# Performance work log

Measured on AMD Instinct MI355X. Metric: run time of the kernel, lower is better.

Reference implementation:

```python
import jax, jax.numpy as jnp
import numpy as np

D_MODEL, NHEAD = 256, 8
HEAD_DIM = D_MODEL // NHEAD  # 32, also the conv group count


def layer_norm(x, w, b, eps=1e-5):
    mu = jnp.mean(x, axis=-1, keepdims=True)
    var = jnp.var(x, axis=-1, keepdims=True)
    return (x - mu) * jax.lax.rsqrt(var + eps) * w + b


def setup_inputs() -> dict:
    key = jax.random.key(0)
    ks = jax.random.split(key, 12)
    b, H, W = 4, 120, 160
    L = H * W  # 19200; 'self' path requires L == H*W
    d, h = D_MODEL, NHEAD
    s = 0.05
    p = lambda i, shape: jax.random.normal(ks[i], shape, jnp.float32) * s
    return {
        "x": jax.random.normal(ks[0], (b, L, d), jnp.float32),
        "source": jax.random.normal(ks[1], (b, L, d), jnp.float32),
        "Wq": p(2, (d, d)), "Wk": p(3, (d, d)), "Wv": p(4, (d, d)),
        "Wmerge": p(5, (d, d)),
        "Wmlp1": p(6, (2 * d, 2 * d)), "Wmlp2": p(7, (2 * d, d)),
        "ln1_w": jnp.ones((d,), jnp.float32), "ln1_b": jnp.zeros((d,), jnp.float32),
        "ln2_w": jnp.ones((d,), jnp.float32), "ln2_b": jnp.zeros((d,), jnp.float32),
        "Wdown": p(8, (2 * d, 64)), "Wup": p(9, (64, d)),
        "fc_w": p(10, (9, 3 * h)), "fc_b": jnp.zeros((9,), jnp.float32),
        "dep_w": p(11, (d, 9, 3, 3)),  # torch OIHW layout, groups=32 (O/g=8, I/g=9)
        "dep_b": jnp.zeros((d,), jnp.float32),
        "rate": jnp.full((1,), 0.5, jnp.float32),
        "H": H, "W": W,
    }


def reference(x, source, Wq, Wk, Wv, Wmerge, Wmlp1, Wmlp2,
              ln1_w, ln1_b, ln2_w, ln2_b, Wdown, Wup,
              fc_w, fc_b, dep_w, dep_b, rate, H, W):
    # name == 'self' path is hardcoded (conv branch active)
    b, L, d = x.shape
    h, hd = NHEAD, HEAD_DIM
    S = source.shape[1]

    q = (x @ Wq).reshape(b, L, h, hd)
    k = (source @ Wk).reshape(b, S, h, hd)
    v = (source @ Wv).reshape(b, S, h, hd)

    # ---- conv branch ----
    # [b, L, h, 3*hd] -> [b, L, 3h, hd] -> [b, 3h, L, hd]
    f_all = jnp.concatenate([q, k, v], axis=-1).reshape(b, L, 3 * h, hd)
    f_all = jnp.transpose(f_all, (0, 2, 1, 3))
    # 1x1 conv 3h -> 9 over (L, hd) 'spatial' grid
    f9 = jnp.einsum('oc,bcld->bold', fc_w, f_all) + fc_b[None, :, None, None]
    # [b, 9, L, hd] -> [b, hd, 9, L] -> [b, 9*hd, H, W]
    f_conv = jnp.transpose(f9, (0, 3, 1, 2)).reshape(b, 9 * hd, H, W)
    out_conv = jax.lax.conv_general_dilated(
        f_conv, dep_w, window_strides=(1, 1), padding=((1, 1), (1, 1)),
        feature_group_count=hd, dimension_numbers=('NCHW', 'OIHW', 'NCHW'))
    out_conv = out_conv + dep_b[None, :, None, None]
    out_conv = jnp.transpose(out_conv, (0, 2, 3, 1)).reshape(b, L, d)

    # ---- linear attention (elu+1 feature map), O(N) ----
    Qf = jax.nn.elu(q) + 1.0
    Kf = jax.nn.elu(k) + 1.0
    v_len = jnp.float32(S)
    vals = v / v_len
    KV = jnp.einsum('bshd,bshv->bhdv', Kf, vals)
    Z = 1.0 / (jnp.einsum('blhd,bhd->blh', Qf, Kf.sum(axis=1)) + 1e-6)
    message = jnp.einsum('blhd,bhdv,blh->blhv', Qf, KV, Z) * v_len

    # ---- merge / norm / MLP / adapter ----
    message = message.reshape(b, L, d) @ Wmerge
    message = layer_norm(message, ln1_w, ln1_b)
    cat1 = jnp.concatenate([x, message], axis=2)
    message = jax.nn.relu(cat1 @ Wmlp1) @ Wmlp2
    message = layer_norm(message, ln2_w, ln2_b)

    cat2 = jnp.concatenate([x, message], axis=2)
    up = jax.nn.relu(cat2 @ Wdown) @ Wup
    message = message + up * 0.1
    message = message + rate * out_conv
    return x + message
```

## Files before the change

kernel.cpp:

```cpp
#include <hip/hip_runtime.h>
#include <stdint.h>

#define LL 19200
#define NBATCH 4
#define NROWS (NBATCH * LL)
#define HH 120
#define WW 160

typedef short bhalf8 __attribute__((ext_vector_type(8)));
typedef float f32x4 __attribute__((ext_vector_type(4)));

__device__ __forceinline__ float bfbits2f(uint32_t u) { union { uint32_t i; float f; } c; c.i = u << 16; return c.f; }
__device__ __forceinline__ float bf2f(uint16_t h) { return bfbits2f((uint32_t)h); }
__device__ __forceinline__ uint16_t f2bf(float f) {
    union { float f; uint32_t i; } c; c.f = f;
    return (uint16_t)((c.i + 0x7FFFu + ((c.i >> 16) & 1u)) >> 16);
}
__device__ __forceinline__ uint32_t pk2(uint16_t a, uint16_t b) { return (uint32_t)a | ((uint32_t)b << 16); }
__device__ __forceinline__ float elup1(float x) { return x > 0.f ? x + 1.f : expf(x); }

__device__ __forceinline__ uint4 pack8f(const float* p) {
    float4 lo = *(const float4*)p; float4 hi = *(const float4*)(p + 4);
    uint4 s;
    s.x = pk2(f2bf(lo.x), f2bf(lo.y)); s.y = pk2(f2bf(lo.z), f2bf(lo.w));
    s.z = pk2(f2bf(hi.x), f2bf(hi.y)); s.w = pk2(f2bf(hi.z), f2bf(hi.w));
    return s;
}

__device__ __forceinline__ void gll16(const void* g, void* l) {
    __builtin_amdgcn_global_load_lds((const __attribute__((address_space(1))) uint32_t*)g,
                                     (__attribute__((address_space(3))) uint32_t*)l, 16, 0, 0);
}

__global__ __launch_bounds__(256)
void prep_all(const float* __restrict__ Wq, const float* __restrict__ Wk,
              const float* __restrict__ Wv, const float* __restrict__ Wm,
              const float* __restrict__ Wm1, const float* __restrict__ Wm2,
              const float* __restrict__ Wd, const float* __restrict__ Wu,
              uint16_t* __restrict__ wq, uint16_t* __restrict__ wk,
              uint16_t* __restrict__ wvv, uint16_t* __restrict__ wm,
              uint16_t* __restrict__ wm1, uint16_t* __restrict__ wm2,
              uint16_t* __restrict__ wd, uint16_t* __restrict__ wu) {
    int blk = blockIdx.x;
    const float* s; uint16_t* d; int K, N, base;
    if (blk < 1024) {
        int which = blk >> 8; base = which << 8;
        s = which == 0 ? Wq : which == 1 ? Wk : which == 2 ? Wv : Wm;
        d = which == 0 ? wq : which == 1 ? wk : which == 2 ? wvv : wm;
        K = 256; N = 256;
    } else if (blk < 2048) { s = Wm1; d = wm1; K = 512; N = 512; base = 1024; }
    else if (blk < 2560)   { s = Wm2; d = wm2; K = 512; N = 256; base = 2048; }
    else if (blk < 2688)   { s = Wd;  d = wd;  K = 512; N = 64;  base = 2560; }
    else                   { s = Wu;  d = wu;  K = 64;  N = 256; base = 2688; }
    int idx = (blk - base) * 256 + threadIdx.x;
    int n = idx / K, kk = idx - n * K;
    d[idx] = f2bf(s[(long)kk * N + n]);
}

#define EPI_NONE 0
#define EPI_RELU 1
#define EPI_LN 2
#define EPI_FINAL 3

template<int BN, int MODE_A, int EPI>
__global__ __launch_bounds__(512)
void gemm_big(const float* __restrict__ A0f, const uint16_t* __restrict__ A0b,
              const uint16_t* __restrict__ A1b,
              const uint16_t* __restrict__ Wt, int K,
              uint16_t* __restrict__ outb, float* __restrict__ outf, int outW,
              uint16_t* __restrict__ sideout,
              const float* __restrict__ lnw, const float* __restrict__ lnb,
              const float* __restrict__ xres, const uint16_t* __restrict__ xresb,
              const uint16_t* __restrict__ msg2res,
              const uint16_t* __restrict__ convres, const float* __restrict__ ratep)
{
    constexpr int WCOLS = BN / 64;
    constexpr int WROWS = 8 / WCOLS;
    constexpr int MT = 128 / (WROWS * 16);
    __shared__ __align__(16) uint16_t a_sm[128 * 32];
    __shared__ __align__(16) uint16_t b_sm[BN * 32];
    const int tid = threadIdx.x;
    const int lane = tid & 63;
    const int wv = tid >> 6;
    const int wr = wv / WCOLS, wc = wv % WCOLS;
    const long row0 = (long)blockIdx.x * 128;
    const int col0 = blockIdx.y * BN;

    f32x4 acc[MT][4];
#pragma unroll
    for (int m = 0; m < MT; ++m)
#pragma unroll
        for (int n = 0; n < 4; ++n) acc[m][n] = (f32x4){0.f, 0.f, 0.f, 0.f};

    const int sr = tid >> 2;
    const int sc = (tid & 3) * 8;
    const long argA = row0 + sr;
    uint16_t* a_dst = a_sm + wv * 512;
    uint16_t* b_dst = b_sm + wv * 512;

    for (int k0 = 0; k0 < K; k0 += 32) {
        if (MODE_A == 0) {
            gll16(A0b + argA * (long)K + k0 + sc, a_dst);
        } else if (MODE_A == 1) {
            uint4 stg = pack8f(A0f + argA * (long)K + k0 + sc);
            *(uint4*)&a_sm[sr * 32 + sc] = stg;
            if (sideout) *(uint4*)(sideout + argA * (long)K + k0 + sc) = stg;
        } else if (MODE_A == 2) {
            if (k0 < 256) *(uint4*)&a_sm[sr * 32 + sc] = pack8f(A0f + argA * 256 + k0 + sc);
            else          gll16(A1b + argA * 256 + (k0 - 256) + sc, a_dst);
        } else {
            const uint16_t* srcp = (k0 < 256) ? (A0b + argA * 256 + k0 + sc)
                                              : (A1b + argA * 256 + (k0 - 256) + sc);
            gll16(srcp, a_dst);
        }
        if (BN == 256) {
            gll16(Wt + (long)(col0 + sr) * K + k0 + sc, b_dst);
            gll16(Wt + (long)(col0 + 128 + sr) * K + k0 + sc, b_sm + 4096 + wv * 512);
        } else {
            if (tid < 256) gll16(Wt + (long)(col0 + sr) * K + k0 + sc, b_dst);
        }
        __syncthreads();
        bhalf8 af[MT];
#pragma unroll
        for (int m = 0; m < MT; ++m)
            af[m] = *(const bhalf8*)&a_sm[(wr * MT * 16 + m * 16 + (lane & 15)) * 32 + (lane >> 4) * 8];
#pragma unroll
        for (int n = 0; n < 4; ++n) {
            bhalf8 bfr = *(const bhalf8*)&b_sm[(wc * 64 + n * 16 + (lane & 15)) * 32 + (lane >> 4) * 8];
#pragma unroll
            for (int m = 0; m < MT; ++m)
                acc[m][n] = __builtin_amdgcn_mfma_f32_16x16x32_bf16(af[m], bfr, acc[m][n], 0, 0, 0);
        }
        __syncthreads();
    }

    const int cl = lane & 15;
    const int rg4 = (lane >> 4) * 4;

    if constexpr (EPI == EPI_LN) {
        __shared__ float red_s[4][128];
        __shared__ float red_ss[4][128];
#pragma unroll
        for (int m = 0; m < MT; ++m)
#pragma unroll
            for (int j = 0; j < 4; ++j) {
                float p = 0.f, pp = 0.f;
#pragma unroll
                for (int n = 0; n < 4; ++n) { float v = acc[m][n][j]; p += v; pp += v * v; }
#pragma unroll
                for (int msk = 1; msk < 16; msk <<= 1) { p += __shfl_xor(p, msk, 64); pp += __shfl_xor(pp, msk, 64); }
                if (cl == 0) {
                    int lr = wr * 64 + m * 16 + rg4 + j;
                    red_s[wc][lr] = p; red_ss[wc][lr] = pp;
                }
            }
        __syncthreads();
#pragma unroll
        for (int m = 0; m < MT; ++m)
#pragma unroll
            for (int j = 0; j < 4; ++j) {
                int lr = wr * 64 + m * 16 + rg4 + j;
                float s = red_s[0][lr] + red_s[1][lr] + red_s[2][lr] + red_s[3][lr];
                float ss = red_ss[0][lr] + red_ss[1][lr] + red_ss[2][lr] + red_ss[3][lr];
                float mu = s * (1.f / 256.f);
                float var = ss * (1.f / 256.f) - mu * mu;
                float rstd = rsqrtf(var + 1e-5f);
                long rowg = row0 + lr;
#pragma unroll
                for (int n = 0; n < 4; ++n) {
                    int col = wc * 64 + n * 16 + cl;
                    float vv = (acc[m][n][j] - mu) * rstd * lnw[col] + lnb[col];
                    outb[rowg * (long)outW + col] = f2bf(vv);
                }
            }
    } else if constexpr (EPI == EPI_FINAL) {
        float rate = ratep[0];
#pragma unroll
        for (int m = 0; m < MT; ++m)
#pragma unroll
            for (int j = 0; j < 4; ++j) {
                long rowg = row0 + wr * MT * 16 + m * 16 + rg4 + j;
                int bb = (int)(rowg / LL);
                int ll = (int)(rowg - (long)bb * LL);
#pragma unroll
                for (int n = 0; n < 4; ++n) {
                    int col = wc * 64 + n * 16 + cl;
                    long o = rowg * 256 + col;
                    float xv = xresb ? bf2f(xresb[o]) : xres[o];
                    float m2 = bf2f(msg2res[o]);
                    float cv = bf2f(convres[((long)(bb * 256 + col)) * LL + ll]);
                    outf[o] = xv + m2 + 0.1f * acc[m][n][j] + rate * cv;
                }
            }
    } else {
#pragma unroll
        for (int m = 0; m < MT; ++m)
#pragma unroll
            for (int j = 0; j < 4; ++j) {
                long rowg = row0 + wr * MT * 16 + m * 16 + rg4 + j;
#pragma unroll
                for (int n = 0; n < 4; ++n) {
                    int col = col0 + wc * 64 + n * 16 + cl;
                    float vv = acc[m][n][j];
                    if (EPI == EPI_RELU) vv = vv > 0.f ? vv : 0.f;
                    outb[rowg * (long)outW + col] = f2bf(vv);
                }
            }
    }
}

__global__ __launch_bounds__(256)
void kv_partial(const uint16_t* __restrict__ kb, const uint16_t* __restrict__ vb,
                float* __restrict__ part) {
    __shared__ float kf_sm[32][33];
    __shared__ float v_sm[32][36];
    const int tid = threadIdx.x;
    const int bh = blockIdx.y, b = bh >> 3, h = bh & 7;
    const int s0 = blockIdx.x * 256;
    const int d = tid >> 3, vg = tid & 7;
    const int sl = tid >> 3, e4 = (tid & 7) * 4;
    float a0 = 0.f, a1 = 0.f, a2 = 0.f, a3 = 0.f, aKs = 0.f;
    for (int it = 0; it < 8; ++it) {
        long base = ((long)(b * LL + s0 + it * 32 + sl)) * 256 + h * 32 + e4;
        uint2 kk = *(const uint2*)(kb + base);
        uint2 vv = *(const uint2*)(vb + base);
        kf_sm[sl][e4 + 0] = elup1(bfbits2f(kk.x & 0xFFFFu));
        kf_sm[sl][e4 + 1] = elup1(bfbits2f(kk.x >> 16));
        kf_sm[sl][e4 + 2] = elup1(bfbits2f(kk.y & 0xFFFFu));
        kf_sm[sl][e4 + 3] = elup1(bfbits2f(kk.y >> 16));
        float4 vf;
        vf.x = bfbits2f(vv.x & 0xFFFFu); vf.y = bfbits2f(vv.x >> 16);
        vf.z = bfbits2f(vv.y & 0xFFFFu); vf.w = bfbits2f(vv.y >> 16);
        *(float4*)&v_sm[sl][e4] = vf;
        __syncthreads();
#pragma unroll 8
        for (int s = 0; s < 32; ++s) {
            float kf = kf_sm[s][d];
            aKs += kf;
            float4 v4 = *(const float4*)&v_sm[s][vg * 4];
            a0 += kf * v4.x; a1 += kf * v4.y; a2 += kf * v4.z; a3 += kf * v4.w;
        }
        __syncthreads();
    }
    long pb = ((long)(blockIdx.x * 32 + bh)) * 1056;
    part[pb + d * 32 + vg * 4 + 0] = a0;
    part[pb + d * 32 + vg * 4 + 1] = a1;
    part[pb + d * 32 + vg * 4 + 2] = a2;
    part[pb + d * 32 + vg * 4 + 3] = a3;
    if (vg == 0) part[pb + 1024 + d] = aKs;
}

__global__ __launch_bounds__(256)
void kv_final(const float* __restrict__ part, float* __restrict__ KVg, float* __restrict__ Ksum) {
    const int bh = blockIdx.x, tid = threadIdx.x;
    for (int idx = tid; idx < 1056; idx += 256) {
        float s = 0.f;
        for (int c = 0; c < 75; ++c) s += part[((long)(c * 32 + bh)) * 1056 + idx];
        if (idx < 1024) KVg[bh * 1024 + idx] = s;
        else Ksum[bh * 32 + idx - 1024] = s;
    }
}

__global__ __launch_bounds__(256)
void attn_mfma(const uint16_t* __restrict__ qb, const float* __restrict__ KVg,
               const float* __restrict__ Ksum, uint16_t* __restrict__ msgout) {
    const int tid = threadIdx.x;
    const int lane = tid & 63;
    const int wv = tid >> 6;
    const long l0 = (long)blockIdx.x * 64;
    const int b = (int)(l0 / LL);
    const int l15 = lane & 15, lk = lane >> 4;
#pragma unroll
    for (int hi = 0; hi < 2; ++hi) {
        const int h = wv * 2 + hi;
        const float* kvb = KVg + ((long)(b * 8 + h)) * 1024;
        const float* ksb = Ksum + (b * 8 + h) * 32;
        bhalf8 B0, B1;
        float ks[8];
#pragma unroll
        for (int i = 0; i < 8; ++i) {
            int k = lk * 8 + i;
            B0[i] = (short)f2bf(kvb[k * 32 + l15]);
            B1[i] = (short)f2bf(kvb[k * 32 + 16 + l15]);
            ks[i] = ksb[k];
        }
#pragma unroll
        for (int rt = 0; rt < 4; ++rt) {
            long row = l0 + rt * 16 + l15;
            uint4 qv = *(const uint4*)(qb + row * 256 + h * 32 + lk * 8);
            float qf[8];
            qf[0] = elup1(bfbits2f(qv.x & 0xFFFFu)); qf[1] = elup1(bfbits2f(qv.x >> 16));
            qf[2] = elup1(bfbits2f(qv.y & 0xFFFFu)); qf[3] = elup1(bfbits2f(qv.y >> 16));
            qf[4] = elup1(bfbits2f(qv.z & 0xFFFFu)); qf[5] = elup1(bfbits2f(qv.z >> 16));
            qf[6] = elup1(bfbits2f(qv.w & 0xFFFFu)); qf[7] = elup1(bfbits2f(qv.w >> 16));
            bhalf8 A;
#pragma unroll
            for (int i = 0; i < 8; ++i) A[i] = (short)f2bf(qf[i]);
            float p = qf[0]*ks[0] + qf[1]*ks[1] + qf[2]*ks[2] + qf[3]*ks[3]
                    + qf[4]*ks[4] + qf[5]*ks[5] + qf[6]*ks[6] + qf[7]*ks[7];
            p += __shfl_xor(p, 16, 64);
            p += __shfl_xor(p, 32, 64);
            f32x4 d0 = (f32x4){0.f,0.f,0.f,0.f}, d1 = (f32x4){0.f,0.f,0.f,0.f};
            d0 = __builtin_amdgcn_mfma_f32_16x16x32_bf16(A, B0, d0, 0, 0, 0);
            d1 = __builtin_amdgcn_mfma_f32_16x16x32_bf16(A, B1, d1, 0, 0, 0);
#pragma unroll
            for (int j = 0; j < 4; ++j) {
                int orl = lk * 4 + j;
                float zr = __shfl(p, orl, 64);
                float Z = 1.f / (zr + 1e-6f);
                long orow = l0 + rt * 16 + orl;
                msgout[orow * 256 + h * 32 + l15]      = f2bf(d0[j] * Z);
                msgout[orow * 256 + h * 32 + 16 + l15] = f2bf(d1[j] * Z);
            }
        }
    }
}

__global__ __launch_bounds__(256)
void f9_kernel(const uint16_t* __restrict__ qb, const uint16_t* __restrict__ kb,
               const uint16_t* __restrict__ vb, const float* __restrict__ fcw,
               const float* __restrict__ fcb, uint16_t* __restrict__ fconv) {
    __shared__ __align__(16) uint16_t sm[3 * 32 * 256];
    char* smb = (char*)sm;
    const int tid = threadIdx.x;
    const int b = blockIdx.y;
    const int l0 = blockIdx.x * 32;
    for (int idx = tid; idx < 3072; idx += 256) {
        int tsr = idx >> 10, row = (idx >> 5) & 31, c = idx & 31;
        const uint16_t* src = tsr == 0 ? qb : (tsr == 1 ? kb : vb);
        uint4 v = *(const uint4*)(src + ((long)(b * LL + l0 + row)) * 256 + c * 8);
        int boff = (c * 16) ^ ((row & 7) << 4);
        *(uint4*)(smb + (tsr * 32 + row) * 512 + boff) = v;
    }
    __syncthreads();
    const int li = tid & 31, g = tid >> 5;
    float acc[9][4];
#pragma unroll
    for (int o = 0; o < 9; ++o) {
        float bv = fcb[o];
#pragma unroll
        for (int j = 0; j < 4; ++j) acc[o][j] = bv;
    }
    const int swz = (li & 7) << 4;
#pragma unroll
    for (int h = 0; h < 8; ++h) {
        float f[3][4];
#pragma unroll
        for (int s = 0; s < 3; ++s) {
            int boff = (h * 64 + g * 8) ^ swz;
            uint2 r = *(const uint2*)(smb + (s * 32 + li) * 512 + boff);
            f[s][0] = bfbits2f(r.x & 0xFFFFu); f[s][1] = bfbits2f(r.x >> 16);
            f[s][2] = bfbits2f(r.y & 0xFFFFu); f[s][3] = bfbits2f(r.y >> 16);
        }
#pragma unroll
        for (int o = 0; o < 9; ++o) {
            float w0 = fcw[o * 24 + 3 * h + 0];
            float w1 = fcw[o * 24 + 3 * h + 1];
            float w2 = fcw[o * 24 + 3 * h + 2];
#pragma unroll
            for (int j = 0; j < 4; ++j)
                acc[o][j] += w0 * f[0][j] + w1 * f[1][j] + w2 * f[2][j];
        }
    }
    const long ob = (long)(b * 288) * LL + l0 + li;
#pragma unroll
    for (int j = 0; j < 4; ++j) {
        int dp = g * 4 + j;
#pragma unroll
        for (int o = 0; o < 9; ++o)
            fconv[ob + (long)(dp * 9 + o) * LL] = f2bf(acc[o][j]);
    }
}

__global__ __launch_bounds__(256)
void dwconv2(const uint16_t* __restrict__ fconv, const float* __restrict__ depw,
             const float* __restrict__ depb, uint16_t* __restrict__ convout) {
    __shared__ __align__(16) uint16_t in_sm[9][26][48];
    __shared__ float w_sm[8][81];
    __shared__ float b_sm2[8];
    const int tid = threadIdx.x;
    const int bg = blockIdx.z, b = bg >> 5, g = bg & 31;
    const int y0 = blockIdx.y * 24;
    const int x0 = blockIdx.x * 32;
    for (int idx = tid; idx < 648; idx += 256)
        w_sm[idx / 81][idx % 81] = depw[(long)(g * 8) * 81 + idx];
    if (tid < 8) b_sm2[tid] = depb[g * 8 + tid];
    for (int rIdx = tid; rIdx < 234; rIdx += 256) {
        int i = rIdx / 26, r = rIdx - i * 26;
        int yy = y0 + r - 1;
        uint16_t* dst = &in_sm[i][r][0];
        if (yy >= 0 && yy < HH) {
            const uint16_t* rp = fconv + ((long)(b * 288 + g * 9 + i)) * LL + yy * WW;
            *(uint4*)&dst[8]  = *(const uint4*)(rp + x0);
            *(uint4*)&dst[16] = *(const uint4*)(rp + x0 + 8);
            *(uint4*)&dst[24] = *(const uint4*)(rp + x0 + 16);
            *(uint4*)&dst[32] = *(const uint4*)(rp + x0 + 24);
            dst[7]  = (x0 > 0) ? rp[x0 - 1] : (uint16_t)0;
            dst[40] = (x0 + 32 < WW) ? rp[x0 + 32] : (uint16_t)0;
        } else {
            uint4 z = {0, 0, 0, 0};
            *(uint4*)&dst[8] = z; *(uint4*)&dst[16] = z;
            *(uint4*)&dst[24] = z; *(uint4*)&dst[32] = z;
            dst[7] = 0; dst[40] = 0;
        }
    }
    __syncthreads();
    const int xi = tid & 7, m = (tid >> 3) & 7, ys = tid >> 6;
    float acc[6][4];
    float bias = b_sm2[m];
#pragma unroll
    for (int r = 0; r < 6; ++r)
#pragma unroll
        for (int o = 0; o < 4; ++o) acc[r][o] = bias;
    for (int i = 0; i < 9; ++i) {
        float w[9];
#pragma unroll
        for (int t = 0; t < 9; ++t) w[t] = w_sm[m][i * 9 + t];
#pragma unroll
        for (int rr = 0; rr < 8; ++rr) {
            const uint16_t* rowb = &in_sm[i][ys * 6 + rr][4 + xi * 4];
            uint2 lo = *(const uint2*)rowb;
            uint2 hi = *(const uint2*)(rowb + 4);
            uint32_t ex = *(const uint32_t*)(rowb + 8);
            float f[6];
            f[0] = bfbits2f(lo.y >> 16);
            f[1] = bfbits2f(hi.x & 0xFFFFu);
            f[2] = bfbits2f(hi.x >> 16);
            f[3] = bfbits2f(hi.y & 0xFFFFu);
            f[4] = bfbits2f(hi.y >> 16);
            f[5] = bfbits2f(ex & 0xFFFFu);
#pragma unroll
            for (int ky = 0; ky < 3; ++ky) {
                int ro = rr - ky;
                if (ro >= 0 && ro < 6) {
#pragma unroll
                    for (int o = 0; o < 4; ++o)
                        acc[ro][o] += w[ky * 3 + 0] * f[o] + w[ky * 3 + 1] * f[o + 1] + w[ky * 3 + 2] * f[o + 2];
                }
            }
        }
    }
    long chbase = ((long)(b * 256 + g * 8 + m)) * LL;
#pragma unroll
    for (int rl = 0; rl < 6; ++rl) {
        int y = y0 + ys * 6 + rl;
        uint2 st;
        st.x = pk2(f2bf(acc[rl][0]), f2bf(acc[rl][1]));
        st.y = pk2(f2bf(acc[rl][2]), f2bf(acc[rl][3]));
        *(uint2*)(convout + chbase + (long)y * WW + x0 + xi * 4) = st;
    }
}

extern "C" void kernel_launch(void* const* d_in, const int* in_sizes, int n_in,
                              void* d_out, int out_size, void* d_ws, size_t ws_size,
                              hipStream_t stream) {
    (void)in_sizes; (void)n_in; (void)out_size;
    const float* x      = (const float*)d_in[0];
    const float* src    = (const float*)d_in[1];
    const float* Wq     = (const float*)d_in[2];
    const float* Wk     = (const float*)d_in[3];
    const float* Wv     = (const float*)d_in[4];
    const float* Wmerge = (const float*)d_in[5];
    const float* Wmlp1  = (const float*)d_in[6];
    const float* Wmlp2  = (const float*)d_in[7];
    const float* ln1w   = (const float*)d_in[8];
    const float* ln1b   = (const float*)d_in[9];
    const float* ln2w   = (const float*)d_in[10];
    const float* ln2b   = (const float*)d_in[11];
    const float* Wdown  = (const float*)d_in[12];
    const float* Wup    = (const float*)d_in[13];
    const float* fcw    = (const float*)d_in[14];
    const float* fcb    = (const float*)d_in[15];
    const float* depw   = (const float*)d_in[16];
    const float* depb   = (const float*)d_in[17];
    const float* rate   = (const float*)d_in[18];

    char* ws = (char*)d_ws;
    const size_t SZ_NB = (size_t)NROWS * 256 * 2;
    const size_t O_Q = 0;
    const size_t O_K = SZ_NB;
    const size_t O_V = 2 * SZ_NB;
    const size_t O_FCONV = 3 * SZ_NB;
    const size_t O_CONVOUT = O_FCONV + (size_t)NBATCH * 288 * LL * 2;
    const size_t O_PART = O_CONVOUT + SZ_NB;
    const size_t O_KV = O_PART + (size_t)75 * 32 * 1056 * 4;
    const size_t O_KS = O_KV + (size_t)32 * 1024 * 4;
    const size_t O_WT = O_KS + (size_t)32 * 32 * 4;
    const size_t O_XB = O_WT + 704512 * 2 + 1024;
    const size_t O_SRCB = O_XB + SZ_NB;
    const size_t NEED = O_SRCB + SZ_NB;

    uint16_t* qB      = (uint16_t*)(ws + O_Q);
    uint16_t* kB      = (uint16_t*)(ws + O_K);
    uint16_t* vB      = (uint16_t*)(ws + O_V);
    uint16_t* fconv   = (uint16_t*)(ws + O_FCONV);
    uint16_t* convout = (uint16_t*)(ws + O_CONVOUT);
    float*    part    = (float*)(ws + O_PART);
    float*    KVg     = (float*)(ws + O_KV);
    float*    Ksg     = (float*)(ws + O_KS);
    uint16_t* wt_q    = (uint16_t*)(ws + O_WT);
    uint16_t* wt_k    = wt_q + 256 * 256;
    uint16_t* wt_v    = wt_k + 256 * 256;
    uint16_t* wt_m    = wt_v + 256 * 256;
    uint16_t* wt_m1   = wt_m + 256 * 256;
    uint16_t* wt_m2   = wt_m1 + 512 * 512;
    uint16_t* wt_d    = wt_m2 + 512 * 256;
    uint16_t* wt_u    = wt_d + 512 * 64;
    uint16_t* xb      = (uint16_t*)(ws + O_XB);
    uint16_t* srcb    = (uint16_t*)(ws + O_SRCB);
    uint16_t* msgattn = kB;
    uint16_t* msgB    = vB;
    uint16_t* hidden  = qB;
    uint16_t* msg2    = fconv;
    uint16_t* h2      = (uint16_t*)(ws + O_PART);

    const bool big = ws_size >= NEED;

    prep_all<<<2752, 256, 0, stream>>>(Wq, Wk, Wv, Wmerge, Wmlp1, Wmlp2, Wdown, Wup,
                                       wt_q, wt_k, wt_v, wt_m, wt_m1, wt_m2, wt_d, wt_u);

    const dim3 g600(NROWS / 128, 1);
    gemm_big<256, 1, EPI_NONE><<<g600, 512, 0, stream>>>(x, nullptr, nullptr, wt_q, 256, qB, nullptr, 256,
        big ? xb : nullptr, nullptr, nullptr, nullptr, nullptr, nullptr, nullptr, nullptr);
    gemm_big<256, 1, EPI_NONE><<<g600, 512, 0, stream>>>(src, nullptr, nullptr, wt_k, 256, kB, nullptr, 256,
        big ? srcb : nullptr, nullptr, nullptr, nullptr, nullptr, nullptr, nullptr, nullptr);
    if (big) {
        gemm_big<256, 0, EPI_NONE><<<g600, 512, 0, stream>>>(nullptr, srcb, nullptr, wt_v, 256, vB, nullptr, 256,
            nullptr, nullptr, nullptr, nullptr, nullptr, nullptr, nullptr, nullptr);
    } else {
        gemm_big<256, 1, EPI_NONE><<<g600, 512, 0, stream>>>(src, nullptr, nullptr, wt_v, 256, vB, nullptr, 256,
            nullptr, nullptr, nullptr, nullptr, nullptr, nullptr, nullptr, nullptr);
    }
    kv_partial<<<dim3(75, 32), 256, 0, stream>>>(kB, vB, part);
    kv_final<<<32, 256, 0, stream>>>(part, KVg, Ksg);
    f9_kernel<<<dim3(LL / 32, NBATCH), 256, 0, stream>>>(qB, kB, vB, fcw, fcb, fconv);
    dwconv2<<<dim3(5, 5, 128), 256, 0, stream>>>(fconv, depw, depb, convout);
    attn_mfma<<<NROWS / 64, 256, 0, stream>>>(qB, KVg, Ksg, msgattn);
    gemm_big<256, 0, EPI_LN><<<g600, 512, 0, stream>>>(nullptr, msgattn, nullptr, wt_m, 256, msgB, nullptr, 256,
        nullptr, ln1w, ln1b, nullptr, nullptr, nullptr, nullptr, nullptr);
    if (big) {
        gemm_big<256, 3, EPI_RELU><<<dim3(NROWS / 128, 2), 512, 0, stream>>>(nullptr, xb, msgB, wt_m1, 512, hidden, nullptr, 512,
            nullptr, nullptr, nullptr, nullptr, nullptr, nullptr, nullptr, nullptr);
    } else {
        gemm_big<256, 2, EPI_RELU><<<dim3(NROWS / 128, 2), 512, 0, stream>>>(x, nullptr, msgB, wt_m1, 512, hidden, nullptr, 512,
            nullptr, nullptr, nullptr, nullptr, nullptr, nullptr, nullptr, nullptr);
    }
    gemm_big<256, 0, EPI_LN><<<g600, 512, 0, stream>>>(nullptr, hidden, nullptr, wt_m2, 512, msg2, nullptr, 256,
        nullptr, ln2w, ln2b, nullptr, nullptr, nullptr, nullptr, nullptr);
    if (big) {
        gemm_big<64, 3, EPI_RELU><<<g600, 512, 0, stream>>>(nullptr, xb, msg2, wt_d, 512, h2, nullptr, 64,
            nullptr, nullptr, nullptr, nullptr, nullptr, nullptr, nullptr, nullptr);
    } else {
        gemm_big<64, 2, EPI_RELU><<<g600, 512, 0, stream>>>(x, nullptr, msg2, wt_d, 512, h2, nullptr, 64,
            nullptr, nullptr, nullptr, nullptr, nullptr, nullptr, nullptr, nullptr);
    }
    gemm_big<256, 0, EPI_FINAL><<<g600, 512, 0, stream>>>(nullptr, h2, nullptr, wt_u, 64, nullptr, (float*)d_out, 256,
        nullptr, nullptr, nullptr, x, big ? xb : nullptr, msg2, convout, rate);
}
```

Measured before the change: 835.3 us.

## Double-buffer GEMM LDS tiles, template K, and tile-transpose weight prep

The GEMM main loop now keeps two LDS buffers, so the next k-slice's global-to-LDS loads are issued before the current slice's MFMAs and one barrier per iteration is removed. K becomes a template parameter so the k-loop can be fully unrolled and address arithmetic folded. Weight preparation switches from a strided per-element transpose over 2752 blocks to a 64x64 shared-memory tiled transpose over 172 blocks, giving coalesced reads and writes. Doubling LDS per block may lower occupancy, and the larger unrolled code may raise register pressure.

```diff
diff --git a/kernel.cpp b/kernel.cpp
--- a/kernel.cpp
+++ b/kernel.cpp
@@ -41,20 +41,32 @@
               uint16_t* __restrict__ wvv, uint16_t* __restrict__ wm,
               uint16_t* __restrict__ wm1, uint16_t* __restrict__ wm2,
               uint16_t* __restrict__ wd, uint16_t* __restrict__ wu) {
+    __shared__ float ts[64][65];
+    const int tid = threadIdx.x;
     int blk = blockIdx.x;
-    const float* s; uint16_t* d; int K, N, base;
-    if (blk < 1024) {
-        int which = blk >> 8; base = which << 8;
-        s = which == 0 ? Wq : which == 1 ? Wk : which == 2 ? Wv : Wm;
-        d = which == 0 ? wq : which == 1 ? wk : which == 2 ? wvv : wm;
-        K = 256; N = 256;
-    } else if (blk < 2048) { s = Wm1; d = wm1; K = 512; N = 512; base = 1024; }
-    else if (blk < 2560)   { s = Wm2; d = wm2; K = 512; N = 256; base = 2048; }
-    else if (blk < 2688)   { s = Wd;  d = wd;  K = 512; N = 64;  base = 2560; }
-    else                   { s = Wu;  d = wu;  K = 64;  N = 256; base = 2688; }
-    int idx = (blk - base) * 256 + threadIdx.x;
-    int n = idx / K, kk = idx - n * K;
-    d[idx] = f2bf(s[(long)kk * N + n]);
+    const float* s; uint16_t* d; int K, N, t;
+    if (blk < 64)        { int w = blk >> 4; t = blk & 15;
+                           s = w == 0 ? Wq : w == 1 ? Wk : w == 2 ? Wv : Wm;
+                           d = w == 0 ? wq : w == 1 ? wk : w == 2 ? wvv : wm;
+                           K = 256; N = 256; }
+    else if (blk < 128)  { s = Wm1; d = wm1; K = 512; N = 512; t = blk - 64; }
+    else if (blk < 160)  { s = Wm2; d = wm2; K = 512; N = 256; t = blk - 128; }
+    else if (blk < 168)  { s = Wd;  d = wd;  K = 512; N = 64;  t = blk - 160; }
+    else                 { s = Wu;  d = wu;  K = 64;  N = 256; t = blk - 168; }
+    const int ntk = K >> 6;
+    const int tn = t / ntk, tk = t - tn * ntk;
+    const int c = tid & 63, r4 = tid >> 6;
+#pragma unroll
+    for (int i = 0; i < 16; ++i) {
+        int r = r4 * 16 + i;
+        ts[r][c] = s[(long)(tk * 64 + r) * N + tn * 64 + c];
+    }
+    __syncthreads();
+#pragma unroll
+    for (int i = 0; i < 16; ++i) {
+        int rr = r4 * 16 + i;
+        d[(long)(tn * 64 + rr) * K + tk * 64 + c] = f2bf(ts[c][rr]);
+    }
 }
 
 #define EPI_NONE 0
@@ -62,11 +74,11 @@
 #define EPI_LN 2
 #define EPI_FINAL 3
 
-template<int BN, int MODE_A, int EPI>
+template<int BN, int K, int MODE_A, int EPI>
 __global__ __launch_bounds__(512)
 void gemm_big(const float* __restrict__ A0f, const uint16_t* __restrict__ A0b,
               const uint16_t* __restrict__ A1b,
-              const uint16_t* __restrict__ Wt, int K,
+              const uint16_t* __restrict__ Wt,
               uint16_t* __restrict__ outb, float* __restrict__ outf, int outW,
               uint16_t* __restrict__ sideout,
               const float* __restrict__ lnw, const float* __restrict__ lnb,
@@ -77,14 +89,17 @@
     constexpr int WCOLS = BN / 64;
     constexpr int WROWS = 8 / WCOLS;
     constexpr int MT = 128 / (WROWS * 16);
-    __shared__ __align__(16) uint16_t a_sm[128 * 32];
-    __shared__ __align__(16) uint16_t b_sm[BN * 32];
+    constexpr int ASZ = 128 * 32;
+    constexpr int BSZ = BN * 32;
+    __shared__ __align__(16) uint16_t a_sm[2 * ASZ];
+    __shared__ __align__(16) uint16_t b_sm[2 * BSZ];
     const int tid = threadIdx.x;
     const int lane = tid & 63;
     const int wv = tid >> 6;
     const int wr = wv / WCOLS, wc = wv % WCOLS;
     const long row0 = (long)blockIdx.x * 128;
     const int col0 = blockIdx.y * BN;
+    const int l15 = lane & 15, lk = lane >> 4;
 
     f32x4 acc[MT][4];
 #pragma unroll
@@ -95,47 +110,62 @@
     const int sr = tid >> 2;
     const int sc = (tid & 3) * 8;
     const long argA = row0 + sr;
-    uint16_t* a_dst = a_sm + wv * 512;
-    uint16_t* b_dst = b_sm + wv * 512;
-
-    for (int k0 = 0; k0 < K; k0 += 32) {
+
+    auto stageAB = [&](int buf, int k0) {
+        uint16_t* ab = a_sm + buf * ASZ;
+        uint16_t* bb = b_sm + buf * BSZ;
         if (MODE_A == 0) {
-            gll16(A0b + argA * (long)K + k0 + sc, a_dst);
+            gll16(A0b + argA * (long)K + k0 + sc, ab + wv * 512);
         } else if (MODE_A == 1) {
             uint4 stg = pack8f(A0f + argA * (long)K + k0 + sc);
-            *(uint4*)&a_sm[sr * 32 + sc] = stg;
+            *(uint4*)&ab[sr * 32 + sc] = stg;
             if (sideout) *(uint4*)(sideout + argA * (long)K + k0 + sc) = stg;
         } else if (MODE_A == 2) {
-            if (k0 < 256) *(uint4*)&a_sm[sr * 32 + sc] = pack8f(A0f + argA * 256 + k0 + sc);
-            else          gll16(A1b + argA * 256 + (k0 - 256) + sc, a_dst);
+            if (k0 < 256) *(uint4*)&ab[sr * 32 + sc] = pack8f(A0f + argA * 256 + k0 + sc);
+            else          gll16(A1b + argA * 256 + (k0 - 256) + sc, ab + wv * 512);
         } else {
             const uint16_t* srcp = (k0 < 256) ? (A0b + argA * 256 + k0 + sc)
                                               : (A1b + argA * 256 + (k0 - 256) + sc);
-            gll16(srcp, a_dst);
+            gll16(srcp, ab + wv * 512);
         }
         if (BN == 256) {
-            gll16(Wt + (long)(col0 + sr) * K + k0 + sc, b_dst);
-            gll16(Wt + (long)(col0 + 128 + sr) * K + k0 + sc, b_sm + 4096 + wv * 512);
+            gll16(Wt + (long)(col0 + sr) * K + k0 + sc, bb + wv * 512);
+            gll16(Wt + (long)(col0 + 128 + sr) * K + k0 + sc, bb + 4096 + wv * 512);
         } else {
-            if (tid < 256) gll16(Wt + (long)(col0 + sr) * K + k0 + sc, b_dst);
-        }
-        __syncthreads();
+            if (tid < 256) gll16(Wt + (long)(col0 + sr) * K + k0 + sc, bb + wv * 512);
+        }
+    };
+
+    auto comp = [&](int buf) {
+        const uint16_t* ab = a_sm + buf * ASZ;
+        const uint16_t* bb = b_sm + buf * BSZ;
         bhalf8 af[MT];
 #pragma unroll
         for (int m = 0; m < MT; ++m)
-            af[m] = *(const bhalf8*)&a_sm[(wr * MT * 16 + m * 16 + (lane & 15)) * 32 + (lane >> 4) * 8];
+            af[m] = *(const bhalf8*)&ab[(wr * MT * 16 + m * 16 + l15) * 32 + lk * 8];
 #pragma unroll
         for (int n = 0; n < 4; ++n) {
-            bhalf8 bfr = *(const bhalf8*)&b_sm[(wc * 64 + n * 16 + (lane & 15)) * 32 + (lane >> 4) * 8];
+            bhalf8 bfr = *(const bhalf8*)&bb[(wc * 64 + n * 16 + l15) * 32 + lk * 8];
 #pragma unroll
             for (int m = 0; m < MT; ++m)
                 acc[m][n] = __builtin_amdgcn_mfma_f32_16x16x32_bf16(af[m], bfr, acc[m][n], 0, 0, 0);
         }
+    };
+
+    stageAB(0, 0);
+    __syncthreads();
+    int cur = 0;
+#pragma unroll
+    for (int k0 = 32; k0 < K; k0 += 32) {
+        stageAB(cur ^ 1, k0);
+        comp(cur);
         __syncthreads();
-    }
-
-    const int cl = lane & 15;
-    const int rg4 = (lane >> 4) * 4;
+        cur ^= 1;
+    }
+    comp(cur);
+
+    const int cl = l15;
+    const int rg4 = lk * 4;
 
     if constexpr (EPI == EPI_LN) {
         __shared__ float red_s[4][128];
@@ -180,15 +210,15 @@
 #pragma unroll
             for (int j = 0; j < 4; ++j) {
                 long rowg = row0 + wr * MT * 16 + m * 16 + rg4 + j;
-                int bb = (int)(rowg / LL);
-                int ll = (int)(rowg - (long)bb * LL);
+                int bb2 = (int)(rowg / LL);
+                int ll = (int)(rowg - (long)bb2 * LL);
 #pragma unroll
                 for (int n = 0; n < 4; ++n) {
                     int col = wc * 64 + n * 16 + cl;
                     long o = rowg * 256 + col;
                     float xv = xresb ? bf2f(xresb[o]) : xres[o];
                     float m2 = bf2f(msg2res[o]);
-                    float cv = bf2f(convres[((long)(bb * 256 + col)) * LL + ll]);
+                    float cv = bf2f(convres[((long)(bb2 * 256 + col)) * LL + ll]);
                     outf[o] = xv + m2 + 0.1f * acc[m][n][j] + rate * cv;
                 }
             }
@@ -516,19 +546,19 @@
 
     const bool big = ws_size >= NEED;
 
-    prep_all<<<2752, 256, 0, stream>>>(Wq, Wk, Wv, Wmerge, Wmlp1, Wmlp2, Wdown, Wup,
-                                       wt_q, wt_k, wt_v, wt_m, wt_m1, wt_m2, wt_d, wt_u);
+    prep_all<<<172, 256, 0, stream>>>(Wq, Wk, Wv, Wmerge, Wmlp1, Wmlp2, Wdown, Wup,
+                                      wt_q, wt_k, wt_v, wt_m, wt_m1, wt_m2, wt_d, wt_u);
 
     const dim3 g600(NROWS / 128, 1);
-    gemm_big<256, 1, EPI_NONE><<<g600, 512, 0, stream>>>(x, nullptr, nullptr, wt_q, 256, qB, nullptr, 256,
+    gemm_big<256, 256, 1, EPI_NONE><<<g600, 512, 0, stream>>>(x, nullptr, nullptr, wt_q, qB, nullptr, 256,
         big ? xb : nullptr, nullptr, nullptr, nullptr, nullptr, nullptr, nullptr, nullptr);
-    gemm_big<256, 1, EPI_NONE><<<g600, 512, 0, stream>>>(src, nullptr, nullptr, wt_k, 256, kB, nullptr, 256,
+    gemm_big<256, 256, 1, EPI_NONE><<<g600, 512, 0, stream>>>(src, nullptr, nullptr, wt_k, kB, nullptr, 256,
         big ? srcb : nullptr, nullptr, nullptr, nullptr, nullptr, nullptr, nullptr, nullptr);
     if (big) {
-        gemm_big<256, 0, EPI_NONE><<<g600, 512, 0, stream>>>(nullptr, srcb, nullptr, wt_v, 256, vB, nullptr, 256,
+        gemm_big<256, 256, 0, EPI_NONE><<<g600, 512, 0, stream>>>(nullptr, srcb, nullptr, wt_v, vB, nullptr, 256,
             nullptr, nullptr, nullptr, nullptr, nullptr, nullptr, nullptr, nullptr);
     } else {
-        gemm_big<256, 1, EPI_NONE><<<g600, 512, 0, stream>>>(src, nullptr, nullptr, wt_v, 256, vB, nullptr, 256,
+        gemm_big<256, 256, 1, EPI_NONE><<<g600, 512, 0, stream>>>(src, nullptr, nullptr, wt_v, vB, nullptr, 256,
             nullptr, nullptr, nullptr, nullptr, nullptr, nullptr, nullptr, nullptr);
     }
     kv_partial<<<dim3(75, 32), 256, 0, stream>>>(kB, vB, part);
@@ -536,24 +566,24 @@
     f9_kernel<<<dim3(LL / 32, NBATCH), 256, 0, stream>>>(qB, kB, vB, fcw, fcb, fconv);
     dwconv2<<<dim3(5, 5, 128), 256, 0, stream>>>(fconv, depw, depb, convout);
     attn_mfma<<<NROWS / 64, 256, 0, stream>>>(qB, KVg, Ksg, msgattn);
-    gemm_big<256, 0, EPI_LN><<<g600, 512, 0, stream>>>(nullptr, msgattn, nullptr, wt_m, 256, msgB, nullptr, 256,
+    gemm_big<256, 256, 0, EPI_LN><<<g600, 512, 0, stream>>>(nullptr, msgattn, nullptr, wt_m, msgB, nullptr, 256,
         nullptr, ln1w, ln1b, nullptr, nullptr, nullptr, nullptr, nullptr);
     if (big) {
-        gemm_big<256, 3, EPI_RELU><<<dim3(NROWS / 128, 2), 512, 0, stream>>>(nullptr, xb, msgB, wt_m1, 512, hidden, nullptr, 512,
+        gemm_big<256, 512, 3, EPI_RELU><<<dim3(NROWS / 128, 2), 512, 0, stream>>>(nullptr, xb, msgB, wt_m1, hidden, nullptr, 512,
             nullptr, nullptr, nullptr, nullptr, nullptr, nullptr, nullptr, nullptr);
     } else {
-        gemm_big<256, 2, EPI_RELU><<<dim3(NROWS / 128, 2), 512, 0, stream>>>(x, nullptr, msgB, wt_m1, 512, hidden, nullptr, 512,
+        gemm_big<256, 512, 2, EPI_RELU><<<dim3(NROWS / 128, 2), 512, 0, stream>>>(x, nullptr, msgB, wt_m1, hidden, nullptr, 512,
             nullptr, nullptr, nullptr, nullptr, nullptr, nullptr, nullptr, nullptr);
     }
-    gemm_big<256, 0, EPI_LN><<<g600, 512, 0, stream>>>(nullptr, hidden, nullptr, wt_m2, 512, msg2, nullptr, 256,
+    gemm_big<256, 512, 0, EPI_LN><<<g600, 512, 0, stream>>>(nullptr, hidden, nullptr, wt_m2, msg2, nullptr, 256,
         nullptr, ln2w, ln2b, nullptr, nullptr, nullptr, nullptr, nullptr);
     if (big) {
-        gemm_big<64, 3, EPI_RELU><<<g600, 512, 0, stream>>>(nullptr, xb, msg2, wt_d, 512, h2, nullptr, 64,
+        gemm_big<64, 512, 3, EPI_RELU><<<g600, 512, 0, stream>>>(nullptr, xb, msg2, wt_d, h2, nullptr, 64,
             nullptr, nullptr, nullptr, nullptr, nullptr, nullptr, nullptr, nullptr);
     } else {
-        gemm_big<64, 2, EPI_RELU><<<g600, 512, 0, stream>>>(x, nullptr, msg2, wt_d, 512, h2, nullptr, 64,
+        gemm_big<64, 512, 2, EPI_RELU><<<g600, 512, 0, stream>>>(x, nullptr, msg2, wt_d, h2, nullptr, 64,
             nullptr, nullptr, nullptr, nullptr, nullptr, nullptr, nullptr, nullptr);
     }
-    gemm_big<256, 0, EPI_FINAL><<<g600, 512, 0, stream>>>(nullptr, h2, nullptr, wt_u, 64, nullptr, (float*)d_out, 256,
+    gemm_big<256, 64, 0, EPI_FINAL><<<g600, 512, 0, stream>>>(nullptr, h2, nullptr, wt_u, nullptr, (float*)d_out, 256,
         nullptr, nullptr, nullptr, x, big ? xb : nullptr, msg2, convout, rate);
 }
```

Measured after the change: 856.3 us. +2.5%, slower.
